# Optimization experiments

Measured on AMD Instinct MI355X. Metric: run time of the kernel, lower is better.

Reference implementation:

```python
import jax, jax.numpy as jnp
import numpy as np

NUM_HEADS = 8

def _spectral_normalize(w, u):
    # One power iteration (power_iterations=1), as in the TF wrapper.
    w2 = w.reshape(-1, w.shape[-1])            # [in, out]
    v = u @ w2.T                               # [1, in]
    v = v / jnp.linalg.norm(v)
    u_new = v @ w2                             # [1, out]
    u_new = u_new / jnp.linalg.norm(u_new)
    sigma = (v @ w2) @ u_new.T                 # [1,1]
    # TF applies normalization by variable assignment (no grad through sigma)
    return w / jax.lax.stop_gradient(sigma[0, 0])

def setup_inputs() -> dict:
    key = jax.random.key(0)
    ks = jax.random.split(key, 14)
    F = 1024
    def dense(k1, k2, k3):
        w = jax.random.normal(k1, (F, F), jnp.float32) * (1.0 / np.sqrt(F))
        b = jnp.zeros((F,), jnp.float32)
        u = jax.random.normal(k3, (1, F), jnp.float32) * 0.02
        return w, b, u
    wq, bq, uq = dense(ks[0], ks[1], ks[2])
    wk, bk, uk = dense(ks[3], ks[4], ks[5])
    wv, bv, uv = dense(ks[6], ks[7], ks[8])
    wo, bo, uo = dense(ks[9], ks[10], ks[11])
    x = jax.random.normal(ks[12], (4, 2048, F), jnp.float32)
    gamma = jnp.array(1.0, jnp.float32)
    return {"x": x, "wq": wq, "bq": bq, "uq": uq, "wk": wk, "bk": bk, "uk": uk,
            "wv": wv, "bv": bv, "uv": uv, "wo": wo, "bo": bo, "uo": uo, "gamma": gamma}

def reference(x, wq, bq, uq, wk, bk, uk, wv, bv, uv, wo, bo, uo, gamma):
    B, S, F = x.shape
    D = F // NUM_HEADS
    def proj(w, b, u):
        return x @ _spectral_normalize(w, u) + b
    def split_heads(t):
        return t.reshape(B, S, NUM_HEADS, D).transpose(0, 2, 1, 3)  # [B,H,S,D]
    q = split_heads(proj(wq, bq, uq))
    k = split_heads(proj(wk, bk, uk))
    v = split_heads(proj(wv, bv, uv))
    # NOTE: original has no 1/sqrt(depth) scaling -- faithful to source.
    logits = jnp.einsum('bhsd,bhtd->bhst', q, k)          # [B,H,S,S]
    attn = jax.nn.softmax(logits, axis=-1)
    ctx = jnp.einsum('bhst,bhtd->bhsd', attn, v)           # [B,H,S,D]
    concat = ctx.transpose(0, 2, 1, 3).reshape(B, S, F)    # merge heads
    # Dropout omitted (deterministic reference / inference mode).
    out = x + (concat @ _spectral_normalize(wo, uo) + bo) * gamma
    return (out, attn)
```

## Files before the change

kernel.cpp:

```cpp
#include <hip/hip_runtime.h>
#include <math.h>

typedef _Float16 h16;
typedef _Float16 half8 __attribute__((ext_vector_type(8)));
typedef _Float16 half4 __attribute__((ext_vector_type(4)));
typedef float floatx4 __attribute__((ext_vector_type(4)));

#define MFMA16(a, b, c) __builtin_amdgcn_mfma_f32_16x16x32_f16(a, b, c, 0, 0, 0)

__device__ __forceinline__ void gload16(const void* g, void* l) {
    __builtin_amdgcn_global_load_lds((const __attribute__((address_space(1))) unsigned int*)g,
                                     (__attribute__((address_space(3))) unsigned int*)l, 16, 0, 0);
}

__global__ void sigma_s1(const float* __restrict__ w0, const float* __restrict__ w1,
                         const float* __restrict__ w2, const float* __restrict__ w3,
                         const float* __restrict__ u0, const float* __restrict__ u1,
                         const float* __restrict__ u2, const float* __restrict__ u3,
                         float* __restrict__ tvec, float* __restrict__ acc) {
    int m = blockIdx.y;
    const float* w = (m == 0) ? w0 : (m == 1) ? w1 : (m == 2) ? w2 : w3;
    const float* u = (m == 0) ? u0 : (m == 1) ? u1 : (m == 2) ? u2 : u3;
    int wid = threadIdx.x >> 6, lane = threadIdx.x & 63;
    int row = blockIdx.x * 4 + wid;
    const float* wr = w + row * 1024;
    float s = 0.f;
    for (int k = 0; k < 16; k++) { int j = lane + 64 * k; s += u[j] * wr[j]; }
    for (int off = 32; off; off >>= 1) s += __shfl_xor(s, off, 64);
    if (lane == 0) { tvec[m * 1024 + row] = s; atomicAdd(acc + m * 2, s * s); }
}

__global__ void sigma_s2(const float* __restrict__ w0, const float* __restrict__ w1,
                         const float* __restrict__ w2, const float* __restrict__ w3,
                         const float* __restrict__ tvec, float* __restrict__ acc) {
    int m = blockIdx.y;
    const float* w = (m == 0) ? w0 : (m == 1) ? w1 : (m == 2) ? w2 : w3;
    const float* t = tvec + m * 1024;
    int j = blockIdx.x * 256 + threadIdx.x;
    float z = 0.f;
    for (int i = 0; i < 1024; i++) z += t[i] * w[i * 1024 + j];
    z = z * z;
    for (int off = 32; off; off >>= 1) z += __shfl_xor(z, off, 64);
    __shared__ float red[4];
    int wid = threadIdx.x >> 6, lane = threadIdx.x & 63;
    if (lane == 0) red[wid] = z;
    __syncthreads();
    if (threadIdx.x == 0) atomicAdd(acc + m * 2 + 1, red[0] + red[1] + red[2] + red[3]);
}

__global__ void sigma_s3(const float* __restrict__ acc, float* __restrict__ inv_sigma) {
    int m = threadIdx.x;
    if (m < 4) inv_sigma[m] = sqrtf(acc[m * 2] / acc[m * 2 + 1]);
}

__global__ void prep_w(const float* __restrict__ w, const float* __restrict__ inv_sigma,
                       int midx, h16* __restrict__ whT, h16* __restrict__ wlT) {
    __shared__ float tile[32][33];
    float is = inv_sigma[midx];
    int i0 = blockIdx.x * 32, j0 = blockIdx.y * 32;
    int tx = threadIdx.x, ty = threadIdx.y;
    for (int r = 0; r < 32; r += 8)
        tile[r + ty][tx] = w[(i0 + r + ty) * 1024 + j0 + tx] * is;
    __syncthreads();
    for (int r = 0; r < 32; r += 8) {
        int j = j0 + r + ty, i = i0 + tx;
        float v = tile[tx][r + ty];
        h16 h = (h16)v;
        whT[j * 1024 + i] = h;
        wlT[j * 1024 + i] = (h16)(v - (float)h);
    }
}

__global__ void prep_x(const float4* __restrict__ x4, half4* __restrict__ xh,
                       half4* __restrict__ xl) {
    int i = blockIdx.x * 256 + threadIdx.x;
    float4 v = x4[i];
    float a[4] = {v.x, v.y, v.z, v.w};
    half4 h, l;
    for (int k = 0; k < 4; k++) {
        h16 hh = (h16)a[k];
        h[k] = hh;
        l[k] = (h16)(a[k] - (float)hh);
    }
    xh[i] = h;
    xl[i] = l;
}

template <int SPLIT>
__global__ __launch_bounds__(256, 2) void gemm_proj(
    const h16* __restrict__ Ah_g, const h16* __restrict__ Al_g,
    const h16* __restrict__ Bh_g, const h16* __restrict__ Bl_g,
    const float* __restrict__ bias, h16* __restrict__ outh, h16* __restrict__ outl) {
    __shared__ h16 As[2][128 * 32];
    __shared__ h16 Bs[2][128 * 32];
    int tid = threadIdx.x;
    int m0 = blockIdx.y * 128, n0 = blockIdx.x * 128;
    int wid = tid >> 6, lane = tid & 63;
    int wm = (wid >> 1) * 64, wn = (wid & 1) * 64;
    int lrow = lane & 15, quad = lane >> 4;
    int srow = lane >> 2;
    int scol = (lane & 3) * 8;
    floatx4 acc[4][4] = {};
    for (int kt = 0; kt < 1024; kt += 32) {
        for (int j = 0; j < 2; j++) {
            int rb = j * 64 + wid * 16;
            int r = rb + srow;
            gload16(&Ah_g[(size_t)(m0 + r) * 1024 + kt + scol], &As[0][rb * 32]);
            gload16(&Bh_g[(size_t)(n0 + r) * 1024 + kt + scol], &Bs[0][rb * 32]);
            if (SPLIT) {
                gload16(&Al_g[(size_t)(m0 + r) * 1024 + kt + scol], &As[1][rb * 32]);
                gload16(&Bl_g[(size_t)(n0 + r) * 1024 + kt + scol], &Bs[1][rb * 32]);
            }
        }
        __syncthreads();
        half8 a_h[4], a_l[4], b_h[4], b_l[4];
        for (int f = 0; f < 4; f++) {
            a_h[f] = *(const half8*)&As[0][(wm + f * 16 + lrow) * 32 + quad * 8];
            b_h[f] = *(const half8*)&Bs[0][(wn + f * 16 + lrow) * 32 + quad * 8];
            if (SPLIT) {
                a_l[f] = *(const half8*)&As[1][(wm + f * 16 + lrow) * 32 + quad * 8];
                b_l[f] = *(const half8*)&Bs[1][(wn + f * 16 + lrow) * 32 + quad * 8];
            }
        }
        for (int mf = 0; mf < 4; mf++)
            for (int nf = 0; nf < 4; nf++) {
                acc[mf][nf] = MFMA16(a_h[mf], b_h[nf], acc[mf][nf]);
                if (SPLIT) {
                    acc[mf][nf] = MFMA16(a_h[mf], b_l[nf], acc[mf][nf]);
                    acc[mf][nf] = MFMA16(a_l[mf], b_h[nf], acc[mf][nf]);
                }
            }
        __syncthreads();
    }
    for (int nf = 0; nf < 4; nf++) {
        int n = n0 + wn + nf * 16 + lrow;
        float b = bias[n];
        int h = n >> 7, d = n & 127;
        for (int mf = 0; mf < 4; mf++)
            for (int r = 0; r < 4; r++) {
                int mg = m0 + wm + mf * 16 + quad * 4 + r;
                int bb = mg >> 11, s = mg & 2047;
                int idx = ((bb * 8 + h) * 2048 + s) * 128 + d;
                float v = acc[mf][nf][r] + b;
                h16 hh = (h16)v;
                outh[idx] = hh;
                if (SPLIT) outl[idx] = (h16)(v - (float)hh);
            }
    }
}

__global__ void transpose_v(const h16* __restrict__ vh, h16* __restrict__ vT) {
    __shared__ h16 tile[32][33];
    int bh = blockIdx.z;
    int t0 = blockIdx.x * 32, d0 = blockIdx.y * 32;
    int tx = threadIdx.x, ty = threadIdx.y;
    const h16* src = vh + bh * 2048 * 128;
    h16* dst = vT + bh * 128 * 2048;
    for (int r = 0; r < 32; r += 8) tile[r + ty][tx] = src[(t0 + r + ty) * 128 + d0 + tx];
    __syncthreads();
    for (int r = 0; r < 32; r += 8) dst[(d0 + r + ty) * 2048 + t0 + tx] = tile[tx][r + ty];
}

__global__ __launch_bounds__(256, 2) void gemm_logits(
    const h16* __restrict__ qh, const h16* __restrict__ ql,
    const h16* __restrict__ kh, const h16* __restrict__ kl, float* __restrict__ attn,
    float* __restrict__ pmax, float* __restrict__ psum) {
    __shared__ h16 As[2][128 * 32];
    __shared__ h16 Bs[2][128 * 32];
    int tid = threadIdx.x;
    int bh = blockIdx.z;
    int s0 = blockIdx.y * 128, t0 = blockIdx.x * 128;
    const h16* Ah_g = qh + bh * 2048 * 128;
    const h16* Al_g = ql + bh * 2048 * 128;
    const h16* Bh_g = kh + bh * 2048 * 128;
    const h16* Bl_g = kl + bh * 2048 * 128;
    int wid = tid >> 6, lane = tid & 63;
    int wm = (wid >> 1) * 64, wn = (wid & 1) * 64;
    int lrow = lane & 15, quad = lane >> 4;
    int srow = lane >> 2;
    int scol = (lane & 3) * 8;
    floatx4 acc[4][4] = {};
    for (int kt = 0; kt < 128; kt += 32) {
        for (int j = 0; j < 2; j++) {
            int rb = j * 64 + wid * 16;
            int r = rb + srow;
            gload16(&Ah_g[(size_t)(s0 + r) * 128 + kt + scol], &As[0][rb * 32]);
            gload16(&Al_g[(size_t)(s0 + r) * 128 + kt + scol], &As[1][rb * 32]);
            gload16(&Bh_g[(size_t)(t0 + r) * 128 + kt + scol], &Bs[0][rb * 32]);
            gload16(&Bl_g[(size_t)(t0 + r) * 128 + kt + scol], &Bs[1][rb * 32]);
        }
        __syncthreads();
        half8 a_h[4], a_l[4], b_h[4], b_l[4];
        for (int f = 0; f < 4; f++) {
            a_h[f] = *(const half8*)&As[0][(wm + f * 16 + lrow) * 32 + quad * 8];
            a_l[f] = *(const half8*)&As[1][(wm + f * 16 + lrow) * 32 + quad * 8];
            b_h[f] = *(const half8*)&Bs[0][(wn + f * 16 + lrow) * 32 + quad * 8];
            b_l[f] = *(const half8*)&Bs[1][(wn + f * 16 + lrow) * 32 + quad * 8];
        }
        for (int mf = 0; mf < 4; mf++)
            for (int nf = 0; nf < 4; nf++) {
                acc[mf][nf] = MFMA16(a_h[mf], b_h[nf], acc[mf][nf]);
                acc[mf][nf] = MFMA16(a_h[mf], b_l[nf], acc[mf][nf]);
                acc[mf][nf] = MFMA16(a_l[mf], b_h[nf], acc[mf][nf]);
            }
        __syncthreads();
    }
    for (int nf = 0; nf < 4; nf++) {
        int t = t0 + wn + nf * 16 + lrow;
        for (int mf = 0; mf < 4; mf++)
            for (int r = 0; r < 4; r++) {
                int s = s0 + wm + mf * 16 + quad * 4 + r;
                attn[((size_t)bh * 2048 + s) * 2048 + t] = acc[mf][nf][r];
            }
    }
    int tile = blockIdx.x * 2 + (wid & 1);
    for (int mf = 0; mf < 4; mf++)
        for (int r = 0; r < 4; r++) {
            float mx = fmaxf(fmaxf(acc[mf][0][r], acc[mf][1][r]),
                             fmaxf(acc[mf][2][r], acc[mf][3][r]));
            for (int off = 8; off; off >>= 1) mx = fmaxf(mx, __shfl_xor(mx, off, 64));
            float z = __expf(acc[mf][0][r] - mx) + __expf(acc[mf][1][r] - mx) +
                      __expf(acc[mf][2][r] - mx) + __expf(acc[mf][3][r] - mx);
            for (int off = 8; off; off >>= 1) z += __shfl_xor(z, off, 64);
            if (lrow == 0) {
                int s = s0 + wm + mf * 16 + quad * 4 + r;
                pmax[((size_t)bh * 2048 + s) * 32 + tile] = mx;
                psum[((size_t)bh * 2048 + s) * 32 + tile] = z;
            }
        }
}

__global__ void combine_stats(const float* __restrict__ pmax, const float* __restrict__ psum,
                              float* __restrict__ m_arr, float* __restrict__ z_arr) {
    int r = blockIdx.x * 256 + threadIdx.x;
    const float* pm = pmax + (size_t)r * 32;
    const float* ps = psum + (size_t)r * 32;
    float m = -1e30f;
    for (int i = 0; i < 32; i++) m = fmaxf(m, pm[i]);
    float z = 0.f;
    for (int i = 0; i < 32; i++) z += ps[i] * __expf(pm[i] - m);
    m_arr[r] = m;
    z_arr[r] = z;
}

__global__ __launch_bounds__(256, 2) void gemm_pv(
    float* __restrict__ attn, const h16* __restrict__ vT, const float* __restrict__ m_arr,
    const float* __restrict__ z_arr, h16* __restrict__ ctx) {
    __shared__ h16 Ps[128 * 72];
    __shared__ h16 Vs[128 * 72];
    __shared__ float ms[128], izs[128];
    int tid = threadIdx.x;
    int bh = blockIdx.y, s0 = blockIdx.x * 128;
    if (tid < 128) ms[tid] = m_arr[bh * 2048 + s0 + tid];
    else izs[tid - 128] = 1.f / z_arr[bh * 2048 + s0 + tid - 128];
    __syncthreads();
    int wid = tid >> 6, lane = tid & 63;
    int wm = (wid >> 1) * 64, wn = (wid & 1) * 64;
    int lrow = lane & 15, quad = lane >> 4;
    float* attn_b = attn + ((size_t)bh * 2048 + s0) * 2048;
    const h16* vT_b = vT + bh * 128 * 2048;
    floatx4 acc[4][4] = {};
    for (int t0 = 0; t0 < 2048; t0 += 64) {
        for (int i = 0; i < 8; i++) {
            int c = tid + 256 * i;
            int row = c >> 4, c4 = c & 15;
            float4* p = (float4*)&attn_b[(size_t)row * 2048 + t0 + c4 * 4];
            float4 l = *p;
            float mm = ms[row], iz = izs[row];
            float4 e;
            e.x = __expf(l.x - mm) * iz;
            e.y = __expf(l.y - mm) * iz;
            e.z = __expf(l.z - mm) * iz;
            e.w = __expf(l.w - mm) * iz;
            *p = e;
            half4 ph;
            ph[0] = (h16)e.x; ph[1] = (h16)e.y; ph[2] = (h16)e.z; ph[3] = (h16)e.w;
            *(half4*)&Ps[row * 72 + c4 * 4] = ph;
        }
        for (int i = 0; i < 4; i++) {
            int c = tid + 256 * i;
            int row = c >> 3, c8 = (c & 7) * 8;
            *(half8*)&Vs[row * 72 + c8] = *(const half8*)&vT_b[row * 2048 + t0 + c8];
        }
        __syncthreads();
        for (int ks = 0; ks < 2; ks++) {
            half8 a[4], b[4];
            for (int f = 0; f < 4; f++) {
                a[f] = *(const half8*)&Ps[(wm + f * 16 + lrow) * 72 + ks * 32 + quad * 8];
                b[f] = *(const half8*)&Vs[(wn + f * 16 + lrow) * 72 + ks * 32 + quad * 8];
            }
            for (int mf = 0; mf < 4; mf++)
                for (int nf = 0; nf < 4; nf++)
                    acc[mf][nf] = MFMA16(a[mf], b[nf], acc[mf][nf]);
        }
        __syncthreads();
    }
    int b = bh >> 3, h = bh & 7;
    for (int nf = 0; nf < 4; nf++) {
        int d = wn + nf * 16 + lrow;
        for (int mf = 0; mf < 4; mf++)
            for (int r = 0; r < 4; r++) {
                int s = s0 + wm + mf * 16 + quad * 4 + r;
                ctx[(b * 2048 + s) * 1024 + h * 128 + d] = (h16)acc[mf][nf][r];
            }
    }
}

__global__ __launch_bounds__(256, 2) void gemm_out(
    const h16* __restrict__ Ah_g, const h16* __restrict__ Bh_g, const float* __restrict__ bo,
    const float* __restrict__ x, const float* __restrict__ gamma_p, float* __restrict__ out) {
    __shared__ h16 As[128 * 32];
    __shared__ h16 Bs[128 * 32];
    int tid = threadIdx.x;
    int m0 = blockIdx.y * 128, n0 = blockIdx.x * 128;
    int wid = tid >> 6, lane = tid & 63;
    int wm = (wid >> 1) * 64, wn = (wid & 1) * 64;
    int lrow = lane & 15, quad = lane >> 4;
    int srow = lane >> 2;
    int scol = (lane & 3) * 8;
    floatx4 acc[4][4] = {};
    for (int kt = 0; kt < 1024; kt += 32) {
        for (int j = 0; j < 2; j++) {
            int rb = j * 64 + wid * 16;
            int r = rb + srow;
            gload16(&Ah_g[(size_t)(m0 + r) * 1024 + kt + scol], &As[rb * 32]);
            gload16(&Bh_g[(size_t)(n0 + r) * 1024 + kt + scol], &Bs[rb * 32]);
        }
        __syncthreads();
        half8 a[4], b[4];
        for (int f = 0; f < 4; f++) {
            a[f] = *(const half8*)&As[(wm + f * 16 + lrow) * 32 + quad * 8];
            b[f] = *(const half8*)&Bs[(wn + f * 16 + lrow) * 32 + quad * 8];
        }
        for (int mf = 0; mf < 4; mf++)
            for (int nf = 0; nf < 4; nf++)
                acc[mf][nf] = MFMA16(a[mf], b[nf], acc[mf][nf]);
        __syncthreads();
    }
    float g = *gamma_p;
    for (int nf = 0; nf < 4; nf++) {
        int n = n0 + wn + nf * 16 + lrow;
        float bb = bo[n];
        for (int mf = 0; mf < 4; mf++)
            for (int r = 0; r < 4; r++) {
                int mg = m0 + wm + mf * 16 + quad * 4 + r;
                out[mg * 1024 + n] = x[mg * 1024 + n] + (acc[mf][nf][r] + bb) * g;
            }
    }
}

extern "C" void kernel_launch(void* const* d_in, const int* in_sizes, int n_in,
                              void* d_out, int out_size, void* d_ws, size_t ws_size,
                              hipStream_t stream) {
    const float* x = (const float*)d_in[0];
    const float* wq = (const float*)d_in[1];
    const float* bq = (const float*)d_in[2];
    const float* uq = (const float*)d_in[3];
    const float* wk = (const float*)d_in[4];
    const float* bk = (const float*)d_in[5];
    const float* uk = (const float*)d_in[6];
    const float* wv = (const float*)d_in[7];
    const float* bv = (const float*)d_in[8];
    const float* uv = (const float*)d_in[9];
    const float* wo = (const float*)d_in[10];
    const float* bo = (const float*)d_in[11];
    const float* uo = (const float*)d_in[12];
    const float* gamma = (const float*)d_in[13];
    float* out_f = (float*)d_out;
    float* attn = out_f + 8388608;

    char* ws = (char*)d_ws;
    size_t o = 0;
    auto alloc = [&](size_t b) { size_t r = o; o += (b + 255) & ~(size_t)255; return r; };
    const size_t SZ_X = (size_t)8192 * 1024 * 2;
    const size_t SZ_W = (size_t)1024 * 1024 * 2;
    const size_t SZ_Q = (size_t)32 * 2048 * 128 * 2;
    h16* xh = (h16*)(ws + alloc(SZ_X));
    h16* xl = (h16*)(ws + alloc(SZ_X));
    h16* wqhT = (h16*)(ws + alloc(SZ_W));
    h16* wqlT = (h16*)(ws + alloc(SZ_W));
    h16* wkhT = (h16*)(ws + alloc(SZ_W));
    h16* wklT = (h16*)(ws + alloc(SZ_W));
    h16* wvhT = (h16*)(ws + alloc(SZ_W));
    h16* wvlT = (h16*)(ws + alloc(SZ_W));
    h16* wohT = (h16*)(ws + alloc(SZ_W));
    h16* wolT = (h16*)(ws + alloc(SZ_W));
    h16* qh = (h16*)(ws + alloc(SZ_Q));
    h16* ql = (h16*)(ws + alloc(SZ_Q));
    h16* kh = (h16*)(ws + alloc(SZ_Q));
    h16* kl = (h16*)(ws + alloc(SZ_Q));
    h16* vh = (h16*)(ws + alloc(SZ_Q));
    h16* vT = (h16*)(ws + alloc(SZ_Q));
    h16* ctx = (h16*)(ws + alloc(SZ_Q));
    float* tvec = (float*)(ws + alloc(4096 * 4));
    float* sacc = (float*)(ws + alloc(8 * 4));
    float* isig = (float*)(ws + alloc(4 * 4));
    float* m_arr = (float*)(ws + alloc(65536 * 4));
    float* z_arr = (float*)(ws + alloc(65536 * 4));
    float* pmax = (float*)ctx;
    float* psum = pmax + (size_t)65536 * 32;

    (void)hipMemsetAsync(sacc, 0, 8 * 4, stream);
    sigma_s1<<<dim3(256, 4), 256, 0, stream>>>(wq, wk, wv, wo, uq, uk, uv, uo, tvec, sacc);
    sigma_s2<<<dim3(4, 4), 256, 0, stream>>>(wq, wk, wv, wo, tvec, sacc);
    sigma_s3<<<1, 64, 0, stream>>>(sacc, isig);

    prep_w<<<dim3(32, 32), dim3(32, 8), 0, stream>>>(wq, isig, 0, wqhT, wqlT);
    prep_w<<<dim3(32, 32), dim3(32, 8), 0, stream>>>(wk, isig, 1, wkhT, wklT);
    prep_w<<<dim3(32, 32), dim3(32, 8), 0, stream>>>(wv, isig, 2, wvhT, wvlT);
    prep_w<<<dim3(32, 32), dim3(32, 8), 0, stream>>>(wo, isig, 3, wohT, wolT);
    prep_x<<<8192, 256, 0, stream>>>((const float4*)x, (half4*)xh, (half4*)xl);

    gemm_proj<1><<<dim3(8, 64), 256, 0, stream>>>(xh, xl, wqhT, wqlT, bq, qh, ql);
    gemm_proj<1><<<dim3(8, 64), 256, 0, stream>>>(xh, xl, wkhT, wklT, bk, kh, kl);
    gemm_proj<0><<<dim3(8, 64), 256, 0, stream>>>(xh, xl, wvhT, wvlT, bv, vh, nullptr);
    transpose_v<<<dim3(64, 4, 32), dim3(32, 8), 0, stream>>>(vh, vT);

    gemm_logits<<<dim3(16, 16, 32), 256, 0, stream>>>(qh, ql, kh, kl, attn, pmax, psum);
    combine_stats<<<256, 256, 0, stream>>>(pmax, psum, m_arr, z_arr);
    gemm_pv<<<dim3(16, 32), 256, 0, stream>>>(attn, vT, m_arr, z_arr, ctx);
    gemm_out<<<dim3(8, 64), 256, 0, stream>>>(ctx, wohT, bo, x, gamma, out_f);

    (void)in_sizes; (void)n_in; (void)out_size; (void)ws_size;
}
```

Measured before the change: 1.467 ms.

## Register-prefetch next attn/V tiles in gemm_pv and raise occupancy hint

The gemm_pv loop now loads the next 64-column tile of attention logits and V into registers while the current tile is normalized and multiplied. This hides global load latency behind the exp/normalize and MFMA work. Per-row max and inverse-sum values are hoisted into registers once, and launch bounds request 3 blocks per CU instead of 2. The prefetch buffers add register pressure, which could conflict with the higher occupancy target and cause spills.

```diff
diff --git a/kernel.cpp b/kernel.cpp
--- a/kernel.cpp
+++ b/kernel.cpp
@@ -243,7 +243,7 @@
     z_arr[r] = z;
 }
 
-__global__ __launch_bounds__(256, 2) void gemm_pv(
+__global__ __launch_bounds__(256, 3) void gemm_pv(
     float* __restrict__ attn, const h16* __restrict__ vT, const float* __restrict__ m_arr,
     const float* __restrict__ z_arr, h16* __restrict__ ctx) {
     __shared__ h16 Ps[128 * 72];
@@ -253,38 +253,56 @@
     int bh = blockIdx.y, s0 = blockIdx.x * 128;
     if (tid < 128) ms[tid] = m_arr[bh * 2048 + s0 + tid];
     else izs[tid - 128] = 1.f / z_arr[bh * 2048 + s0 + tid - 128];
-    __syncthreads();
     int wid = tid >> 6, lane = tid & 63;
     int wm = (wid >> 1) * 64, wn = (wid & 1) * 64;
     int lrow = lane & 15, quad = lane >> 4;
     float* attn_b = attn + ((size_t)bh * 2048 + s0) * 2048;
     const h16* vT_b = vT + bh * 128 * 2048;
+    int prow = tid >> 4, pc4 = (tid & 15) * 4;
+    int vrow = tid >> 3, vc8 = (tid & 7) * 8;
+    __syncthreads();
+    float mm[8], iz[8];
+#pragma unroll
+    for (int i = 0; i < 8; i++) { mm[i] = ms[prow + 16 * i]; iz[i] = izs[prow + 16 * i]; }
+    float4 preP[8];
+    half8 preV[4];
+#pragma unroll
+    for (int i = 0; i < 8; i++)
+        preP[i] = *(const float4*)&attn_b[(size_t)(prow + 16 * i) * 2048 + pc4];
+#pragma unroll
+    for (int i = 0; i < 4; i++)
+        preV[i] = *(const half8*)&vT_b[(vrow + 32 * i) * 2048 + vc8];
     floatx4 acc[4][4] = {};
     for (int t0 = 0; t0 < 2048; t0 += 64) {
+#pragma unroll
         for (int i = 0; i < 8; i++) {
-            int c = tid + 256 * i;
-            int row = c >> 4, c4 = c & 15;
-            float4* p = (float4*)&attn_b[(size_t)row * 2048 + t0 + c4 * 4];
-            float4 l = *p;
-            float mm = ms[row], iz = izs[row];
+            float4 l = preP[i];
             float4 e;
-            e.x = __expf(l.x - mm) * iz;
-            e.y = __expf(l.y - mm) * iz;
-            e.z = __expf(l.z - mm) * iz;
-            e.w = __expf(l.w - mm) * iz;
-            *p = e;
+            e.x = __expf(l.x - mm[i]) * iz[i];
+            e.y = __expf(l.y - mm[i]) * iz[i];
+            e.z = __expf(l.z - mm[i]) * iz[i];
+            e.w = __expf(l.w - mm[i]) * iz[i];
+            *(float4*)&attn_b[(size_t)(prow + 16 * i) * 2048 + t0 + pc4] = e;
             half4 ph;
             ph[0] = (h16)e.x; ph[1] = (h16)e.y; ph[2] = (h16)e.z; ph[3] = (h16)e.w;
-            *(half4*)&Ps[row * 72 + c4 * 4] = ph;
-        }
-        for (int i = 0; i < 4; i++) {
-            int c = tid + 256 * i;
-            int row = c >> 3, c8 = (c & 7) * 8;
-            *(half8*)&Vs[row * 72 + c8] = *(const half8*)&vT_b[row * 2048 + t0 + c8];
-        }
-        __syncthreads();
+            *(half4*)&Ps[(prow + 16 * i) * 72 + pc4] = ph;
+        }
+#pragma unroll
+        for (int i = 0; i < 4; i++)
+            *(half8*)&Vs[(vrow + 32 * i) * 72 + vc8] = preV[i];
+        if (t0 + 64 < 2048) {
+#pragma unroll
+            for (int i = 0; i < 8; i++)
+                preP[i] = *(const float4*)&attn_b[(size_t)(prow + 16 * i) * 2048 + t0 + 64 + pc4];
+#pragma unroll
+            for (int i = 0; i < 4; i++)
+                preV[i] = *(const half8*)&vT_b[(vrow + 32 * i) * 2048 + t0 + 64 + vc8];
+        }
+        __syncthreads();
+#pragma unroll
         for (int ks = 0; ks < 2; ks++) {
             half8 a[4], b[4];
+#pragma unroll
             for (int f = 0; f < 4; f++) {
                 a[f] = *(const half8*)&Ps[(wm + f * 16 + lrow) * 72 + ks * 32 + quad * 8];
                 b[f] = *(const half8*)&Vs[(wn + f * 16 + lrow) * 72 + ks * 32 + quad * 8];
```

Result: faster. 1.386 ms (-5.5%).
